# Kernel optimization log

Hardware: AMD Instinct MI355X
Metric: run time of the kernel (lower is better)

Reference implementation:

```python
import jax, jax.numpy as jnp
import numpy as np

B, C, D, H, W = 2, 64, 3, 96, 96
CD = C * D  # conv1x1 channel count = in_dim * 3


def setup_inputs() -> dict:
    key = jax.random.key(0)
    ks = jax.random.split(key, 7)
    s = 1.0 / np.sqrt(CD)
    x = jax.random.normal(ks[0], (B, C, D, H, W), dtype=jnp.float32)
    Wq = jax.random.uniform(ks[1], (CD, CD), jnp.float32, -s, s)
    bq = jax.random.uniform(ks[2], (CD,), jnp.float32, -s, s)
    Wk = jax.random.uniform(ks[3], (CD, CD), jnp.float32, -s, s)
    bk = jax.random.uniform(ks[4], (CD,), jnp.float32, -s, s)
    Wv = jax.random.uniform(ks[5], (CD, CD), jnp.float32, -s, s)
    bv = jax.random.uniform(ks[6], (CD,), jnp.float32, -s, s)
    return {"x": x, "Wq": Wq, "bq": bq, "Wk": Wk, "bk": bk, "Wv": Wv, "bv": bv}


def reference(x, Wq, bq, Wk, bk, Wv, bv):
    b, c, d, h, w = x.shape
    n = h * w
    xr = x.reshape(b, c * d, n)  # [B, CD, N]; conv1x1 == channel matmul
    q = jnp.einsum('oc,bcn->bon', Wq, xr) + bq[:, None]  # [B, CD, N]
    k = jnp.einsum('oc,bcn->bon', Wk, xr) + bk[:, None]
    v = jnp.einsum('oc,bcn->bon', Wv, xr) + bv[:, None]
    energy = jnp.einsum('bcn,bcm->bnm', q, k)            # [B, N, N]
    attention = jax.nn.softmax(energy, axis=-1)
    # out = bmm(value, attention^T): out[b,c,m] = sum_n v[b,c,n] * attn[b,m,n]
    out = jnp.einsum('bcn,bmn->bcm', v, attention)       # [B, CD, N]
    return out.reshape(b, c, d, h, w)
```

## Files before the change

kernel.cpp:

```cpp
#include <hip/hip_runtime.h>

#define NSEQ  9216
#define CDIM  192
#define LOG2E 1.44269504088896f

typedef _Float16 h8_t  __attribute__((ext_vector_type(8)));
typedef _Float16 h4_t  __attribute__((ext_vector_type(4)));
typedef _Float16 h2_t  __attribute__((ext_vector_type(2)));
typedef __fp16   fp16x2 __attribute__((ext_vector_type(2)));
typedef float    f4_t  __attribute__((ext_vector_type(4)));
typedef float    f16v  __attribute__((ext_vector_type(16)));
typedef unsigned u32x2 __attribute__((ext_vector_type(2)));

static __device__ inline unsigned f2u(float f) { union { float f; unsigned u; } x; x.f = f; return x.u; }
static __device__ inline float u2f(unsigned u) { union { unsigned u; float f; } x; x.u = u; return x.f; }

static __device__ inline unsigned cvt_pk(float a, float b) {
    union { fp16x2 h; unsigned u; } x;
    x.h = __builtin_amdgcn_cvt_pkrtz(a, b);
    return x.u;
}

static __device__ inline u32x2 plswap(unsigned a, unsigned b) {
    return __builtin_amdgcn_permlane32_swap(a, b, false, false);
}

__global__ __launch_bounds__(256) void wconv_kernel(
    const float* __restrict__ Wq, const float* __restrict__ Wk,
    const float* __restrict__ Wv, _Float16* __restrict__ Wh)
{
    int i = blockIdx.x * 256 + threadIdx.x;
    if (i >= 3 * 9216) return;
    const float* src = (i < 9216) ? Wq : (i < 18432 ? Wk : Wv);
    float s = (i < 9216) ? LOG2E : 1.f;
    int r = i % 9216;
    f4_t w = ((const f4_t*)src)[r];
    h4_t h = {(_Float16)(w[0]*s), (_Float16)(w[1]*s),
              (_Float16)(w[2]*s), (_Float16)(w[3]*s)};
    ((h4_t*)Wh)[i] = h;
}

__global__ __launch_bounds__(384) void proj_kernel(
    const float* __restrict__ x, const _Float16* __restrict__ Wh,
    const float* __restrict__ bq, const float* __restrict__ bk,
    const float* __restrict__ bv,
    _Float16* __restrict__ QT, _Float16* __restrict__ KT, _Float16* __restrict__ Vg)
{
    __shared__ __align__(16) _Float16 Xs[32 * 200];

    const int tid  = threadIdx.x;
    const int lane = tid & 63, wave = tid >> 6;
    const int L31  = lane & 31, hi = lane >> 5;
    const int b    = blockIdx.x / 288;
    const int n0   = (blockIdx.x % 288) * 32;

    {
        const int nn = tid & 31;
        const int c0 = (tid >> 5) * 16;
        const float* xp = x + (size_t)(b * CDIM + c0) * NSEQ + n0 + nn;
        _Float16 tmp[16];
        #pragma unroll
        for (int j = 0; j < 16; j++)
            tmp[j] = (_Float16)xp[(size_t)j * NSEQ];
        #pragma unroll
        for (int g = 0; g < 4; g++) {
            h4_t h = {tmp[4*g], tmp[4*g+1], tmp[4*g+2], tmp[4*g+3]};
            *(h4_t*)(Xs + nn * 200 + c0 + 4 * g) = h;
        }
    }
    __syncthreads();

    const int mat = wave >> 1;
    const int sh  = (wave & 1) * 3;
    const int n   = n0 + L31;

    h8_t bf[12];
    #pragma unroll
    for (int t = 0; t < 12; t++)
        bf[t] = *(const h8_t*)(Xs + L31 * 200 + t * 16 + hi * 8);

    const _Float16* W = Wh + mat * CDIM * CDIM;
    const float* bias = (mat == 0) ? bq : (mat == 1 ? bk : bv);
    const float bscale = (mat == 0) ? LOG2E : 1.f;

    f16v acc[3];
    #pragma unroll
    for (int s = 0; s < 3; s++)
        #pragma unroll
        for (int r = 0; r < 16; r++) acc[s][r] = 0.f;

    __builtin_amdgcn_s_setprio(1);
    #pragma unroll
    for (int t = 0; t < 12; t++) {
        #pragma unroll
        for (int s = 0; s < 3; s++) {
            h8_t a = *(const h8_t*)(W + ((sh + s) * 32 + L31) * CDIM + t * 16 + hi * 8);
            acc[s] = __builtin_amdgcn_mfma_f32_32x32x16_f16(a, bf[t], acc[s], 0, 0, 0);
        }
    }
    __builtin_amdgcn_s_setprio(0);

    if (mat < 2) {
        _Float16* dst = ((mat == 0) ? QT : KT) + ((size_t)b * NSEQ + n) * CDIM;
        #pragma unroll
        for (int s = 0; s < 3; s++) {
            #pragma unroll
            for (int g = 0; g < 4; g++) {
                f4_t bb = *(const f4_t*)&bias[(sh + s) * 32 + 8 * g + 4 * hi];
                h4_t h = {(_Float16)(acc[s][4*g+0] + bb[0] * bscale),
                          (_Float16)(acc[s][4*g+1] + bb[1] * bscale),
                          (_Float16)(acc[s][4*g+2] + bb[2] * bscale),
                          (_Float16)(acc[s][4*g+3] + bb[3] * bscale)};
                *(h4_t*)(dst + (sh + s) * 32 + 8 * g + 4 * hi) = h;
            }
        }
    } else {
        #pragma unroll
        for (int s = 0; s < 3; s++) {
            #pragma unroll
            for (int g = 0; g < 4; g++) {
                f4_t bb = *(const f4_t*)&bias[(sh + s) * 32 + 8 * g + 4 * hi];
                #pragma unroll
                for (int r = 0; r < 4; r++) {
                    int o = (sh + s) * 32 + 8 * g + 4 * hi + r;
                    Vg[((size_t)b * CDIM + o) * NSEQ + n] =
                        (_Float16)(acc[s][4*g+r] + bb[r]);
                }
            }
        }
    }
}

template<int NSPLIT>
__global__ __launch_bounds__(256, 2) void flash_kernel(
    const _Float16* __restrict__ QT, const _Float16* __restrict__ KTg,
    const _Float16* __restrict__ Vg,
    _Float16* __restrict__ O_part, float* __restrict__ m_part, float* __restrict__ l_part)
{
    constexpr int KPS    = NSEQ / NSPLIT;
    constexpr int KITERS = KPS / 32;
    constexpr int KBUF   = 32 * 200;
    constexpr int DBUF   = 14080;
    __shared__ __align__(16) _Float16 Sh[2 * DBUF];

    const int tid  = threadIdx.x;
    const int lane = tid & 63, wave = tid >> 6;
    const int L31  = lane & 31, hi = lane >> 5;
    const int qtile = blockIdx.x, split = blockIdx.y, b = blockIdx.z;
    const int q0 = qtile * 128 + wave * 32;

    h8_t qf[12];
    const _Float16* qbase = QT + ((size_t)b * NSEQ + q0 + L31) * CDIM + hi * 8;
    #pragma unroll
    for (int t = 0; t < 12; t++) qf[t] = *(const h8_t*)(qbase + t * 16);

    f16v acc[6];
    #pragma unroll
    for (int s = 0; s < 6; s++)
        #pragma unroll
        for (int r = 0; r < 16; r++) acc[s][r] = 0.f;
    float m_run = -__builtin_inff();
    float l_run = 0.f;

    const _Float16* ksrc = KTg + ((size_t)b * NSEQ + split * KPS) * CDIM;
    const _Float16* vsrc = Vg + (size_t)b * CDIM * NSEQ + split * KPS;

    int kds[3], vds[3];
    const _Float16 *kgl[3], *vgl[3];
    #pragma unroll
    for (int r = 0; r < 3; r++) {
        int i = r * 256 + tid;
        kds[r] = (i / 24) * 200 + (i % 24) * 8;
        kgl[r] = ksrc + i * 8;
        int c = i >> 2, seg = i & 3;
        vds[r] = KBUF + c * 40 + seg * 8;
        vgl[r] = vsrc + (size_t)c * NSEQ + seg * 8;
    }

    h8_t kreg[3], vreg[3];
    #pragma unroll
    for (int r = 0; r < 3; r++) kreg[r] = *(const h8_t*)(kgl[r]);
    #pragma unroll
    for (int r = 0; r < 3; r++) vreg[r] = *(const h8_t*)(vgl[r]);
    #pragma unroll
    for (int r = 0; r < 3; r++) *(h8_t*)(Sh + kds[r]) = kreg[r];
    #pragma unroll
    for (int r = 0; r < 3; r++) *(h8_t*)(Sh + vds[r]) = vreg[r];
    if (KITERS > 1) {
        #pragma unroll
        for (int r = 0; r < 3; r++) kreg[r] = *(const h8_t*)(kgl[r] + 32 * CDIM);
        #pragma unroll
        for (int r = 0; r < 3; r++) vreg[r] = *(const h8_t*)(vgl[r] + 32);
    }
    __syncthreads();

    for (int kt = 0; kt < KITERS; kt++) {
        const int rb = (kt & 1) * DBUF;
        const int wb = ((kt + 1) & 1) * DBUF;

        if (kt + 1 < KITERS) {
            #pragma unroll
            for (int r = 0; r < 3; r++) *(h8_t*)(Sh + wb + kds[r]) = kreg[r];
            #pragma unroll
            for (int r = 0; r < 3; r++) *(h8_t*)(Sh + wb + vds[r]) = vreg[r];
        }
        if (kt + 2 < KITERS) {
            #pragma unroll
            for (int r = 0; r < 3; r++)
                kreg[r] = *(const h8_t*)(kgl[r] + (kt + 2) * 32 * CDIM);
            #pragma unroll
            for (int r = 0; r < 3; r++)
                vreg[r] = *(const h8_t*)(vgl[r] + (kt + 2) * 32);
        }

        f16v st;
        #pragma unroll
        for (int r = 0; r < 16; r++) st[r] = 0.f;
        __builtin_amdgcn_s_setprio(1);
        #pragma unroll
        for (int t = 0; t < 12; t++) {
            h8_t a = *(const h8_t*)(Sh + rb + L31 * 200 + t * 16 + hi * 8);
            st = __builtin_amdgcn_mfma_f32_32x32x16_f16(a, qf[t], st, 0, 0, 0);
        }
        __builtin_amdgcn_s_setprio(0);

        float a0 = fmaxf(fmaxf(st[0], st[1]),  st[2]);
        float a1 = fmaxf(fmaxf(st[3], st[4]),  st[5]);
        float a2 = fmaxf(fmaxf(st[6], st[7]),  st[8]);
        float a3 = fmaxf(fmaxf(st[9], st[10]), st[11]);
        float a4 = fmaxf(fmaxf(st[12], st[13]), st[14]);
        float mx = fmaxf(fmaxf(fmaxf(a0, a1), fmaxf(a2, a3)), fmaxf(a4, st[15]));
        u32x2 mxw = plswap(f2u(mx), f2u(mx));
        mx = fmaxf(u2f(mxw[0]), u2f(mxw[1]));

        if (__builtin_expect(__any(mx > m_run + 9.f), 0)) {
            float m_new = fmaxf(m_run, mx);
            float alpha = __builtin_exp2f(m_run - m_new);
            l_run *= alpha;
            #pragma unroll
            for (int cs = 0; cs < 6; cs++)
                #pragma unroll
                for (int r = 0; r < 16; r++) acc[cs][r] *= alpha;
            m_run = m_new;
        }

        unsigned pu[8];
        float ps0 = 0.f, ps1 = 0.f;
        #pragma unroll
        for (int t2 = 0; t2 < 8; t2++) {
            float e0 = __builtin_exp2f(st[2*t2]   - m_run);
            float e1 = __builtin_exp2f(st[2*t2+1] - m_run);
            ps0 += e0; ps1 += e1;
            pu[t2] = cvt_pk(e0, e1);
        }
        l_run += ps0 + ps1;

        union { h8_t h; unsigned u[4]; } pb0, pb1;
        u32x2 x0 = plswap(pu[0], pu[2]);
        u32x2 x1 = plswap(pu[1], pu[3]);
        u32x2 x2 = plswap(pu[4], pu[6]);
        u32x2 x3 = plswap(pu[5], pu[7]);
        pb0.u[0] = x0[0]; pb0.u[1] = x1[0]; pb0.u[2] = x0[1]; pb0.u[3] = x1[1];
        pb1.u[0] = x2[0]; pb1.u[1] = x3[0]; pb1.u[2] = x2[1]; pb1.u[3] = x3[1];

        __builtin_amdgcn_s_setprio(1);
        #pragma unroll
        for (int ks = 0; ks < 2; ks++) {
            h8_t pb = ks ? pb1.h : pb0.h;
            #pragma unroll
            for (int cs = 0; cs < 6; cs++) {
                h8_t va = *(const h8_t*)(Sh + rb + KBUF + (cs * 32 + L31) * 40 + ks * 16 + hi * 8);
                acc[cs] = __builtin_amdgcn_mfma_f32_32x32x16_f16(va, pb, acc[cs], 0, 0, 0);
            }
        }
        __builtin_amdgcn_s_setprio(0);

        __syncthreads();
    }

    u32x2 lw = plswap(f2u(l_run), f2u(l_run));
    float l_tot = u2f(lw[0]) + u2f(lw[1]);
    const size_t pw = (size_t)(b * NSPLIT + split) * NSEQ + q0;
    if (lane < 32) {
        m_part[pw + lane] = m_run;
        l_part[pw + lane] = l_tot;
    }
    _Float16* T = Sh + wave * 6400;
    #pragma unroll
    for (int cs = 0; cs < 6; cs++)
        #pragma unroll
        for (int g = 0; g < 4; g++) {
            h4_t hh = {(_Float16)acc[cs][4*g+0], (_Float16)acc[cs][4*g+1],
                       (_Float16)acc[cs][4*g+2], (_Float16)acc[cs][4*g+3]};
            *(h4_t*)(T + L31 * 200 + cs * 32 + 8 * g + 4 * hi) = hh;
        }
    _Float16* ob = O_part + pw * CDIM;
    #pragma unroll
    for (int it = 0; it < 12; it++) {
        int i = it * 64 + lane;
        int qq = i / 24, col = i % 24;
        h8_t h = *(const h8_t*)(T + qq * 200 + col * 8);
        *(h8_t*)(ob + (size_t)qq * CDIM + col * 8) = h;
    }
}

template<int NS>
__global__ __launch_bounds__(256) void combine_kernel(
    const _Float16* __restrict__ O_part, const float* __restrict__ m_part,
    const float* __restrict__ l_part, float* __restrict__ out)
{
    __shared__ float Cs[CDIM][33];
    __shared__ float winv[NS][32];
    const int tid = threadIdx.x;
    const int b  = blockIdx.y;
    const int n0 = blockIdx.x * 32;

    if (tid < 32) {
        int n = n0 + tid;
        float mm[NS], ll[NS], ms = -__builtin_inff();
        #pragma unroll
        for (int s = 0; s < NS; s++) {
            mm[s] = m_part[(b * NS + s) * NSEQ + n];
            ll[s] = l_part[(b * NS + s) * NSEQ + n];
            ms = fmaxf(ms, mm[s]);
        }
        float denom = 0.f;
        #pragma unroll
        for (int s = 0; s < NS; s++) {
            float w = __builtin_exp2f(mm[s] - ms);
            mm[s] = w;
            denom += w * ll[s];
        }
        #pragma unroll
        for (int s = 0; s < NS; s++) winv[s][tid] = mm[s] / denom;
    }
    __syncthreads();

    for (int i = tid; i < 32 * 24; i += 256) {
        int nl = i / 24, cp = i % 24;
        float v[8];
        #pragma unroll
        for (int j = 0; j < 8; j++) v[j] = 0.f;
        #pragma unroll
        for (int s = 0; s < NS; s++) {
            h8_t op = *(const h8_t*)(O_part +
                ((size_t)(b * NS + s) * NSEQ + n0 + nl) * CDIM + cp * 8);
            float w = winv[s][nl];
            #pragma unroll
            for (int j = 0; j < 8; j++) v[j] += w * (float)op[j];
        }
        #pragma unroll
        for (int j = 0; j < 8; j++) Cs[cp * 8 + j][nl] = v[j];
    }
    __syncthreads();
    for (int i = tid; i < CDIM * 32; i += 256) {
        int nl = i & 31, c = i >> 5;
        out[((size_t)b * CDIM + c) * NSEQ + n0 + nl] = Cs[c][nl];
    }
}

extern "C" void kernel_launch(void* const* d_in, const int* in_sizes, int n_in,
                              void* d_out, int out_size, void* d_ws, size_t ws_size,
                              hipStream_t stream)
{
    const float* x  = (const float*)d_in[0];
    const float* Wq = (const float*)d_in[1];
    const float* bq = (const float*)d_in[2];
    const float* Wk = (const float*)d_in[3];
    const float* bk = (const float*)d_in[4];
    const float* Wv = (const float*)d_in[5];
    const float* bv = (const float*)d_in[6];
    float* out = (float*)d_out;

    char* ws = (char*)d_ws;
    _Float16* QT = (_Float16*)(ws);
    _Float16* KT = (_Float16*)(ws + 7077888);
    _Float16* Vg = (_Float16*)(ws + 14155776);
    char* tail = ws + 21233664;
    _Float16* Wh = (_Float16*)tail;
    _Float16* O_part = (_Float16*)tail;

    wconv_kernel<<<108, 256, 0, stream>>>(Wq, Wk, Wv, Wh);
    proj_kernel<<<576, 384, 0, stream>>>(x, Wh, bq, bk, bv, QT, KT, Vg);

    const size_t need8 = 21233664ull + 8 * 7077888ull + 2 * 589824ull;
    const size_t need4 = 21233664ull + 4 * 7077888ull + 2 * 294912ull;
    if (ws_size >= need8) {
        float* m_part = (float*)(tail + 8 * 7077888ull);
        float* l_part = (float*)(tail + 8 * 7077888ull + 589824ull);
        flash_kernel<8><<<dim3(72, 8, 2), 256, 0, stream>>>(QT, KT, Vg, O_part, m_part, l_part);
        combine_kernel<8><<<dim3(288, 2), 256, 0, stream>>>(O_part, m_part, l_part, out);
    } else if (ws_size >= need4) {
        float* m_part = (float*)(tail + 4 * 7077888ull);
        float* l_part = (float*)(tail + 4 * 7077888ull + 294912ull);
        flash_kernel<4><<<dim3(72, 4, 2), 256, 0, stream>>>(QT, KT, Vg, O_part, m_part, l_part);
        combine_kernel<4><<<dim3(288, 2), 256, 0, stream>>>(O_part, m_part, l_part, out);
    } else {
        float* m_part = (float*)(tail + 2 * 7077888ull);
        float* l_part = (float*)(tail + 2 * 7077888ull + 147456ull);
        flash_kernel<2><<<dim3(72, 2, 2), 256, 0, stream>>>(QT, KT, Vg, O_part, m_part, l_part);
        combine_kernel<2><<<dim3(288, 2), 256, 0, stream>>>(O_part, m_part, l_part, out);
    }
}
```

Baseline: 299.8 us.

## Software-pipeline QK^T of next tile with softmax and PV of previous tile

Restructures the flash attention loop so each iteration computes the S=K·Q MFMA tile for the current key block while running softmax and the P·V MFMAs for the previous block, using a triple-buffered V tile in shared memory and double-buffered K. An epilogue handles the final block. It also removes the s_setprio priority hints in both the projection and flash kernels. The goal is to let the exp/max VALU work overlap with matrix-core work within a wave. In exchange it holds an extra 16-float score register set and uses more LDS, which may hurt occupancy at the stated 2 blocks per CU.

```diff
diff --git a/kernel.cpp b/kernel.cpp
--- a/kernel.cpp
+++ b/kernel.cpp
@@ -89,7 +89,6 @@
         #pragma unroll
         for (int r = 0; r < 16; r++) acc[s][r] = 0.f;
 
-    __builtin_amdgcn_s_setprio(1);
     #pragma unroll
     for (int t = 0; t < 12; t++) {
         #pragma unroll
@@ -98,7 +97,6 @@
             acc[s] = __builtin_amdgcn_mfma_f32_32x32x16_f16(a, bf[t], acc[s], 0, 0, 0);
         }
     }
-    __builtin_amdgcn_s_setprio(0);
 
     if (mat < 2) {
         _Float16* dst = ((mat == 0) ? QT : KT) + ((size_t)b * NSEQ + n) * CDIM;
@@ -139,9 +137,12 @@
 {
     constexpr int KPS    = NSEQ / NSPLIT;
     constexpr int KITERS = KPS / 32;
-    constexpr int KBUF   = 32 * 200;
-    constexpr int DBUF   = 14080;
-    __shared__ __align__(16) _Float16 Sh[2 * DBUF];
+    static_assert(KITERS % 3 == 0, "V3 epilogue slot assumption");
+    constexpr int KROW   = 200;
+    constexpr int KTILE  = 32 * KROW;
+    constexpr int VTILE  = 192 * 40;
+    constexpr int VBASE  = 2 * KTILE;
+    __shared__ __align__(16) _Float16 Sh[VBASE + 3 * VTILE];
 
     const int tid  = threadIdx.x;
     const int lane = tid & 63, wave = tid >> 6;
@@ -170,10 +171,10 @@
     #pragma unroll
     for (int r = 0; r < 3; r++) {
         int i = r * 256 + tid;
-        kds[r] = (i / 24) * 200 + (i % 24) * 8;
+        kds[r] = (i / 24) * KROW + (i % 24) * 8;
         kgl[r] = ksrc + i * 8;
         int c = i >> 2, seg = i & 3;
-        vds[r] = KBUF + c * 40 + seg * 8;
+        vds[r] = c * 40 + seg * 8;
         vgl[r] = vsrc + (size_t)c * NSEQ + seg * 8;
     }
 
@@ -185,7 +186,7 @@
     #pragma unroll
     for (int r = 0; r < 3; r++) *(h8_t*)(Sh + kds[r]) = kreg[r];
     #pragma unroll
-    for (int r = 0; r < 3; r++) *(h8_t*)(Sh + vds[r]) = vreg[r];
+    for (int r = 0; r < 3; r++) *(h8_t*)(Sh + VBASE + vds[r]) = vreg[r];
     if (KITERS > 1) {
         #pragma unroll
         for (int r = 0; r < 3; r++) kreg[r] = *(const h8_t*)(kgl[r] + 32 * CDIM);
@@ -194,15 +195,30 @@
     }
     __syncthreads();
 
+    f16v stp;
+    #pragma unroll
+    for (int r = 0; r < 16; r++) stp[r] = 0.f;
+    int vw = 1;
+    int vr = 2;
+
     for (int kt = 0; kt < KITERS; kt++) {
-        const int rb = (kt & 1) * DBUF;
-        const int wb = ((kt + 1) & 1) * DBUF;
+        const int kb  = (kt & 1) * KTILE;
+        const int kbw = ((kt + 1) & 1) * KTILE;
+
+        f16v st;
+        #pragma unroll
+        for (int r = 0; r < 16; r++) st[r] = 0.f;
+        #pragma unroll
+        for (int t = 0; t < 12; t++) {
+            h8_t a = *(const h8_t*)(Sh + kb + L31 * KROW + t * 16 + hi * 8);
+            st = __builtin_amdgcn_mfma_f32_32x32x16_f16(a, qf[t], st, 0, 0, 0);
+        }
 
         if (kt + 1 < KITERS) {
             #pragma unroll
-            for (int r = 0; r < 3; r++) *(h8_t*)(Sh + wb + kds[r]) = kreg[r];
-            #pragma unroll
-            for (int r = 0; r < 3; r++) *(h8_t*)(Sh + wb + vds[r]) = vreg[r];
+            for (int r = 0; r < 3; r++) *(h8_t*)(Sh + kbw + kds[r]) = kreg[r];
+            #pragma unroll
+            for (int r = 0; r < 3; r++) *(h8_t*)(Sh + VBASE + vw * VTILE + vds[r]) = vreg[r];
         }
         if (kt + 2 < KITERS) {
             #pragma unroll
@@ -213,27 +229,76 @@
                 vreg[r] = *(const h8_t*)(vgl[r] + (kt + 2) * 32);
         }
 
-        f16v st;
-        #pragma unroll
-        for (int r = 0; r < 16; r++) st[r] = 0.f;
-        __builtin_amdgcn_s_setprio(1);
-        #pragma unroll
-        for (int t = 0; t < 12; t++) {
-            h8_t a = *(const h8_t*)(Sh + rb + L31 * 200 + t * 16 + hi * 8);
-            st = __builtin_amdgcn_mfma_f32_32x32x16_f16(a, qf[t], st, 0, 0, 0);
-        }
-        __builtin_amdgcn_s_setprio(0);
-
-        float a0 = fmaxf(fmaxf(st[0], st[1]),  st[2]);
-        float a1 = fmaxf(fmaxf(st[3], st[4]),  st[5]);
-        float a2 = fmaxf(fmaxf(st[6], st[7]),  st[8]);
-        float a3 = fmaxf(fmaxf(st[9], st[10]), st[11]);
-        float a4 = fmaxf(fmaxf(st[12], st[13]), st[14]);
-        float mx = fmaxf(fmaxf(fmaxf(a0, a1), fmaxf(a2, a3)), fmaxf(a4, st[15]));
+        if (kt > 0) {
+            float a0 = fmaxf(fmaxf(stp[0], stp[1]),  stp[2]);
+            float a1 = fmaxf(fmaxf(stp[3], stp[4]),  stp[5]);
+            float a2 = fmaxf(fmaxf(stp[6], stp[7]),  stp[8]);
+            float a3 = fmaxf(fmaxf(stp[9], stp[10]), stp[11]);
+            float a4 = fmaxf(fmaxf(stp[12], stp[13]), stp[14]);
+            float mx = fmaxf(fmaxf(fmaxf(a0, a1), fmaxf(a2, a3)), fmaxf(a4, stp[15]));
+            u32x2 mxw = plswap(f2u(mx), f2u(mx));
+            mx = fmaxf(u2f(mxw[0]), u2f(mxw[1]));
+
+            if (__builtin_expect(__any(mx > m_run + 9.f), 0)) {
+                float m_new = fmaxf(m_run, mx);
+                float alpha = __builtin_exp2f(m_run - m_new);
+                l_run *= alpha;
+                #pragma unroll
+                for (int cs = 0; cs < 6; cs++)
+                    #pragma unroll
+                    for (int r = 0; r < 16; r++) acc[cs][r] *= alpha;
+                m_run = m_new;
+            }
+
+            unsigned pu[8];
+            float ps0 = 0.f, ps1 = 0.f;
+            #pragma unroll
+            for (int t2 = 0; t2 < 8; t2++) {
+                float e0 = __builtin_exp2f(stp[2*t2]   - m_run);
+                float e1 = __builtin_exp2f(stp[2*t2+1] - m_run);
+                ps0 += e0; ps1 += e1;
+                pu[t2] = cvt_pk(e0, e1);
+            }
+            l_run += ps0 + ps1;
+
+            union { h8_t h; unsigned u[4]; } pb0, pb1;
+            u32x2 x0 = plswap(pu[0], pu[2]);
+            u32x2 x1 = plswap(pu[1], pu[3]);
+            u32x2 x2 = plswap(pu[4], pu[6]);
+            u32x2 x3 = plswap(pu[5], pu[7]);
+            pb0.u[0] = x0[0]; pb0.u[1] = x1[0]; pb0.u[2] = x0[1]; pb0.u[3] = x1[1];
+            pb1.u[0] = x2[0]; pb1.u[1] = x3[0]; pb1.u[2] = x2[1]; pb1.u[3] = x3[1];
+
+            const int vb = VBASE + vr * VTILE;
+            #pragma unroll
+            for (int ks = 0; ks < 2; ks++) {
+                h8_t pb = ks ? pb1.h : pb0.h;
+                #pragma unroll
+                for (int cs = 0; cs < 6; cs++) {
+                    h8_t va = *(const h8_t*)(Sh + vb + (cs * 32 + L31) * 40 + ks * 16 + hi * 8);
+                    acc[cs] = __builtin_amdgcn_mfma_f32_32x32x16_f16(va, pb, acc[cs], 0, 0, 0);
+                }
+            }
+        }
+
+        stp = st;
+        vw = (vw == 2) ? 0 : vw + 1;
+        vr = (vr == 2) ? 0 : vr + 1;
+        __syncthreads();
+    }
+
+    {
+        constexpr int VEPI = (KITERS - 1) % 3;
+        float a0 = fmaxf(fmaxf(stp[0], stp[1]),  stp[2]);
+        float a1 = fmaxf(fmaxf(stp[3], stp[4]),  stp[5]);
+        float a2 = fmaxf(fmaxf(stp[6], stp[7]),  stp[8]);
+        float a3 = fmaxf(fmaxf(stp[9], stp[10]), stp[11]);
+        float a4 = fmaxf(fmaxf(stp[12], stp[13]), stp[14]);
+        float mx = fmaxf(fmaxf(fmaxf(a0, a1), fmaxf(a2, a3)), fmaxf(a4, stp[15]));
         u32x2 mxw = plswap(f2u(mx), f2u(mx));
         mx = fmaxf(u2f(mxw[0]), u2f(mxw[1]));
 
-        if (__builtin_expect(__any(mx > m_run + 9.f), 0)) {
+        if (__any(mx > m_run + 9.f)) {
             float m_new = fmaxf(m_run, mx);
             float alpha = __builtin_exp2f(m_run - m_new);
             l_run *= alpha;
@@ -248,8 +313,8 @@
         float ps0 = 0.f, ps1 = 0.f;
         #pragma unroll
         for (int t2 = 0; t2 < 8; t2++) {
-            float e0 = __builtin_exp2f(st[2*t2]   - m_run);
-            float e1 = __builtin_exp2f(st[2*t2+1] - m_run);
+            float e0 = __builtin_exp2f(stp[2*t2]   - m_run);
+            float e1 = __builtin_exp2f(stp[2*t2+1] - m_run);
             ps0 += e0; ps1 += e1;
             pu[t2] = cvt_pk(e0, e1);
         }
@@ -263,19 +328,16 @@
         pb0.u[0] = x0[0]; pb0.u[1] = x1[0]; pb0.u[2] = x0[1]; pb0.u[3] = x1[1];
         pb1.u[0] = x2[0]; pb1.u[1] = x3[0]; pb1.u[2] = x2[1]; pb1.u[3] = x3[1];
 
-        __builtin_amdgcn_s_setprio(1);
+        const int vb = VBASE + VEPI * VTILE;
         #pragma unroll
         for (int ks = 0; ks < 2; ks++) {
             h8_t pb = ks ? pb1.h : pb0.h;
             #pragma unroll
             for (int cs = 0; cs < 6; cs++) {
-                h8_t va = *(const h8_t*)(Sh + rb + KBUF + (cs * 32 + L31) * 40 + ks * 16 + hi * 8);
+                h8_t va = *(const h8_t*)(Sh + vb + (cs * 32 + L31) * 40 + ks * 16 + hi * 8);
                 acc[cs] = __builtin_amdgcn_mfma_f32_32x32x16_f16(va, pb, acc[cs], 0, 0, 0);
             }
         }
-        __builtin_amdgcn_s_setprio(0);
-
-        __syncthreads();
     }
 
     u32x2 lw = plswap(f2u(l_run), f2u(l_run));
```

New measurement: 291.8 us. -2.7%, faster.

## Stage K/V tiles via direct global-to-LDS loads with swizzled layout

Applied to the files above, without the earlier changes.

Replaces the register-staged double-buffer (global load to registers, then LDS store) with global_load_lds direct-to-LDS transfers, using an XOR/rotation swizzle in place of padded rows to avoid bank conflicts. The kt loop is unrolled by two so buffer offsets become compile-time constants, and the setprio hints around the MFMA blocks are removed. This aims to cut VGPR pressure and the VALU/LDS-store instructions spent on staging, at the cost of relying on the async LDS load completing before the barrier and on the new address mapping being correct.

```diff
diff --git a/kernel.cpp b/kernel.cpp
--- a/kernel.cpp
+++ b/kernel.cpp
@@ -23,6 +23,13 @@
 
 static __device__ inline u32x2 plswap(unsigned a, unsigned b) {
     return __builtin_amdgcn_permlane32_swap(a, b, false, false);
+}
+
+static __device__ inline void gl_lds16(const _Float16* g, _Float16* l) {
+    __builtin_amdgcn_global_load_lds(
+        (const __attribute__((address_space(1))) void*)g,
+        (__attribute__((address_space(3))) void*)l,
+        16, 0, 0);
 }
 
 __global__ __launch_bounds__(256) void wconv_kernel(
@@ -89,7 +96,6 @@
         #pragma unroll
         for (int r = 0; r < 16; r++) acc[s][r] = 0.f;
 
-    __builtin_amdgcn_s_setprio(1);
     #pragma unroll
     for (int t = 0; t < 12; t++) {
         #pragma unroll
@@ -98,7 +104,6 @@
             acc[s] = __builtin_amdgcn_mfma_f32_32x32x16_f16(a, bf[t], acc[s], 0, 0, 0);
         }
     }
-    __builtin_amdgcn_s_setprio(0);
 
     if (mat < 2) {
         _Float16* dst = ((mat == 0) ? QT : KT) + ((size_t)b * NSEQ + n) * CDIM;
@@ -139,9 +144,8 @@
 {
     constexpr int KPS    = NSEQ / NSPLIT;
     constexpr int KITERS = KPS / 32;
-    constexpr int KBUF   = 32 * 200;
-    constexpr int DBUF   = 14080;
-    __shared__ __align__(16) _Float16 Sh[2 * DBUF];
+    static_assert(KITERS % 2 == 0, "kt loop unrolled by 2");
+    __shared__ __align__(16) _Float16 Sh[25600];
 
     const int tid  = threadIdx.x;
     const int lane = tid & 63, wave = tid >> 6;
@@ -165,64 +169,53 @@
     const _Float16* ksrc = KTg + ((size_t)b * NSEQ + split * KPS) * CDIM;
     const _Float16* vsrc = Vg + (size_t)b * CDIM * NSEQ + split * KPS;
 
-    int kds[3], vds[3];
-    const _Float16 *kgl[3], *vgl[3];
+    const int k7 = L31 & 7;
+    int ka[12];
+    #pragma unroll
+    for (int t = 0; t < 12; t++) {
+        int p = 2 * t + hi + k7; if (p >= 24) p -= 24;
+        ka[t] = L31 * 384 + p * 16;
+    }
+    const int va0 = L31 * 64 + ((hi + L31) & 3) * 16;
+    const int va1 = L31 * 64 + ((2 + hi + L31) & 3) * 16;
+
+    const _Float16 *kp[3], *vp[3];
     #pragma unroll
     for (int r = 0; r < 3; r++) {
         int i = r * 256 + tid;
-        kds[r] = (i / 24) * 200 + (i % 24) * 8;
-        kgl[r] = ksrc + i * 8;
-        int c = i >> 2, seg = i & 3;
-        vds[r] = KBUF + c * 40 + seg * 8;
-        vgl[r] = vsrc + (size_t)c * NSEQ + seg * 8;
-    }
-
-    h8_t kreg[3], vreg[3];
-    #pragma unroll
-    for (int r = 0; r < 3; r++) kreg[r] = *(const h8_t*)(kgl[r]);
-    #pragma unroll
-    for (int r = 0; r < 3; r++) vreg[r] = *(const h8_t*)(vgl[r]);
-    #pragma unroll
-    for (int r = 0; r < 3; r++) *(h8_t*)(Sh + kds[r]) = kreg[r];
-    #pragma unroll
-    for (int r = 0; r < 3; r++) *(h8_t*)(Sh + vds[r]) = vreg[r];
-    if (KITERS > 1) {
-        #pragma unroll
-        for (int r = 0; r < 3; r++) kreg[r] = *(const h8_t*)(kgl[r] + 32 * CDIM);
-        #pragma unroll
-        for (int r = 0; r < 3; r++) vreg[r] = *(const h8_t*)(vgl[r] + 32);
-    }
+        int row = i / 24, pp = i % 24;
+        int c = pp - (row & 7); if (c < 0) c += 24;
+        kp[r] = ksrc + row * CDIM + c * 8;
+        int cv = i >> 2, s = i & 3;
+        int g = (s - cv) & 3;
+        vp[r] = vsrc + (size_t)cv * NSEQ + g * 8;
+    }
+
+    auto stage = [&](int kbB, int vbB) {
+        #pragma unroll
+        for (int r = 0; r < 3; r++) {
+            int off = (r * 256 + wave * 64) * 16;
+            gl_lds16(kp[r], (_Float16*)((char*)Sh + kbB + off));
+            gl_lds16(vp[r], (_Float16*)((char*)Sh + vbB + off));
+        }
+        #pragma unroll
+        for (int r = 0; r < 3; r++) { kp[r] += 32 * CDIM; vp[r] += 32; }
+    };
+
+    stage(0, 24576);
     __syncthreads();
 
-    for (int kt = 0; kt < KITERS; kt++) {
-        const int rb = (kt & 1) * DBUF;
-        const int wb = ((kt + 1) & 1) * DBUF;
-
-        if (kt + 1 < KITERS) {
-            #pragma unroll
-            for (int r = 0; r < 3; r++) *(h8_t*)(Sh + wb + kds[r]) = kreg[r];
-            #pragma unroll
-            for (int r = 0; r < 3; r++) *(h8_t*)(Sh + wb + vds[r]) = vreg[r];
-        }
-        if (kt + 2 < KITERS) {
-            #pragma unroll
-            for (int r = 0; r < 3; r++)
-                kreg[r] = *(const h8_t*)(kgl[r] + (kt + 2) * 32 * CDIM);
-            #pragma unroll
-            for (int r = 0; r < 3; r++)
-                vreg[r] = *(const h8_t*)(vgl[r] + (kt + 2) * 32);
-        }
+    auto body = [&](int kt, int KB, int VB, int KW, int VW) {
+        if (kt + 1 < KITERS) stage(KW, VW);
 
         f16v st;
         #pragma unroll
         for (int r = 0; r < 16; r++) st[r] = 0.f;
-        __builtin_amdgcn_s_setprio(1);
         #pragma unroll
         for (int t = 0; t < 12; t++) {
-            h8_t a = *(const h8_t*)(Sh + rb + L31 * 200 + t * 16 + hi * 8);
+            h8_t a = *(const h8_t*)((char*)Sh + KB + ka[t]);
             st = __builtin_amdgcn_mfma_f32_32x32x16_f16(a, qf[t], st, 0, 0, 0);
         }
-        __builtin_amdgcn_s_setprio(0);
 
         float a0 = fmaxf(fmaxf(st[0], st[1]),  st[2]);
         float a1 = fmaxf(fmaxf(st[3], st[4]),  st[5]);
@@ -263,19 +256,23 @@
         pb0.u[0] = x0[0]; pb0.u[1] = x1[0]; pb0.u[2] = x0[1]; pb0.u[3] = x1[1];
         pb1.u[0] = x2[0]; pb1.u[1] = x3[0]; pb1.u[2] = x2[1]; pb1.u[3] = x3[1];
 
-        __builtin_amdgcn_s_setprio(1);
         #pragma unroll
         for (int ks = 0; ks < 2; ks++) {
             h8_t pb = ks ? pb1.h : pb0.h;
+            int vaof = ks ? va1 : va0;
             #pragma unroll
             for (int cs = 0; cs < 6; cs++) {
-                h8_t va = *(const h8_t*)(Sh + rb + KBUF + (cs * 32 + L31) * 40 + ks * 16 + hi * 8);
+                h8_t va = *(const h8_t*)((char*)Sh + VB + cs * 2048 + vaof);
                 acc[cs] = __builtin_amdgcn_mfma_f32_32x32x16_f16(va, pb, acc[cs], 0, 0, 0);
             }
         }
-        __builtin_amdgcn_s_setprio(0);
 
         __syncthreads();
+    };
+
+    for (int kt = 0; kt < KITERS; kt += 2) {
+        body(kt,     0,     24576, 12288, 36864);
+        body(kt + 1, 12288, 36864, 0,     24576);
     }
 
     u32x2 lw = plswap(f2u(l_run), f2u(l_run));
```

Measured after the change: 290.5 us. -3.1%, faster.
